# Performance work log

Hardware: AMD Instinct MI355X
Metric: run time of the kernel (lower is better)

Reference implementation:

```python
import jax, jax.numpy as jnp
import numpy as np

B, S, E, H = 256, 64, 256, 8
d = E // H          # qkv_size per head = 32
D = S * d           # flattened per-head linear dim = 2048


def setup_inputs() -> dict:
    key = jax.random.key(0)
    ks = jax.random.split(key, 8)
    w_scale = 1.0 / np.sqrt(D).astype(np.float32)
    return {
        "basic_decoder_out": jax.random.normal(ks[0], (B, S, E), dtype=jnp.float32),
        "final_encoder_out": jax.random.normal(ks[1], (B, S, E), dtype=jnp.float32),
        # stacked per-head Linear params: weight [H, D_out, D_in], bias [H, D_out]
        "WQ": jax.random.normal(ks[2], (H, D, D), dtype=jnp.float32) * w_scale,
        "bQ": jax.random.normal(ks[3], (H, D), dtype=jnp.float32) * w_scale,
        "WK": jax.random.normal(ks[4], (H, D, D), dtype=jnp.float32) * w_scale,
        "bK": jax.random.normal(ks[5], (H, D), dtype=jnp.float32) * w_scale,
        "WV": jax.random.normal(ks[6], (H, D, D), dtype=jnp.float32) * w_scale,
        "bV": jax.random.normal(ks[7], (H, D), dtype=jnp.float32) * w_scale,
    }


def _split_heads_flat(x):
    # [B, S, E] -> [H, B, S*d]: slice head channels, flatten (seq, qkv) per head
    b, s, e = x.shape
    return x.reshape(b, s, H, d).transpose(2, 0, 1, 3).reshape(H, b, s * d)


def reference(basic_decoder_out, final_encoder_out, WQ, bQ, WK, bK, WV, bV):
    b = basic_decoder_out.shape[0]
    xd = _split_heads_flat(basic_decoder_out)   # [H, B, D]
    xe = _split_heads_flat(final_encoder_out)   # [H, B, D]

    # per-head Linear over flattened (seq*qkv): y = x @ W^T + b
    Q = (jnp.einsum('hbi,hoi->hbo', xd, WQ) + bQ[:, None, :]).reshape(H, b, S, d)
    K = (jnp.einsum('hbi,hoi->hbo', xe, WK) + bK[:, None, :]).reshape(H, b, S, d)
    V = (jnp.einsum('hbi,hoi->hbo', xe, WV) + bV[:, None, :]).reshape(H, b, S, d)

    scores = jnp.einsum('hbqd,hbkd->hbqk', Q, K)        # [H, B, Sq, Sk]
    # original uses nn.Softmax(dim=1) on [B, Sq, Sk] -> softmax over QUERY axis
    attn = jax.nn.softmax(scores, axis=2)
    Z = jnp.einsum('hbqk,hbkd->hbqd', attn, V)
    Z = Z * np.float32(1.0 / np.sqrt(d))                # scale applied AFTER attn@V

    # concat heads: [H, B, S, d] -> [B, S, H*d]
    return Z.transpose(1, 2, 0, 3).reshape(b, S, H * d)
```

## Files before the change

### kernel.cpp

```cpp
#include <hip/hip_runtime.h>
#include <hip/hip_fp16.h>

#define HH 8
#define BB 256
#define SS 64
#define EE 256
#define DH 32
#define DD 2048

typedef _Float16 f16x8 __attribute__((ext_vector_type(8)));
typedef _Float16 f16x4 __attribute__((ext_vector_type(4)));
typedef float f32x4v __attribute__((ext_vector_type(4)));

#define BM 256
#define BN 128
#define BK 64
#define LDK 72

__global__ __launch_bounds__(512, 4)
void qkv_kernel(const float* __restrict__ dec, const float* __restrict__ enc,
                const float* __restrict__ WQ, const float* __restrict__ bQ,
                const float* __restrict__ WK, const float* __restrict__ bK,
                const float* __restrict__ WV, const float* __restrict__ bV,
                __half* __restrict__ qkv)
{
    __shared__ _Float16 Asm[BM][LDK];
    __shared__ _Float16 Bsm[BN][LDK];

    const int z = blockIdx.z;
    const int p = z >> 3;
    const int h = z & 7;
    const float* __restrict__ x    = (p == 0) ? dec : enc;
    const float* __restrict__ W    = (p == 0) ? WQ : (p == 1) ? WK : WV;
    const float* __restrict__ bias = (p == 0) ? bQ : (p == 1) ? bK : bV;
    const float* __restrict__ Wh = W + (size_t)h * DD * DD;
    const float* __restrict__ bh = bias + h * DD;
    const int n0 = blockIdx.x * BN;

    const int tid  = threadIdx.x;
    const int lane = tid & 63;
    const int wave = tid >> 6;
    const int wm = wave & 3;
    const int wn = wave >> 2;

    f32x4v acc[4][4];
    #pragma unroll
    for (int m = 0; m < 4; ++m)
        #pragma unroll
        for (int n = 0; n < 4; ++n)
            acc[m][n] = (f32x4v){0.f, 0.f, 0.f, 0.f};

    const int rrow = lane & 15;
    const int kg   = lane >> 4;

    for (int k0 = 0; k0 < DD; k0 += BK) {
        #pragma unroll
        for (int r = 0; r < 8; ++r) {
            int g   = r * 512 + tid;
            int row = g >> 4;
            int k   = (g & 15) * 4;
            const float4 v = *(const float4*)(x + (size_t)row * (SS * EE)
                                + ((k0 + k) >> 5) * EE + h * DH + (k & 31));
            f16x4 hv = { (_Float16)v.x, (_Float16)v.y, (_Float16)v.z, (_Float16)v.w };
            *(f16x4*)&Asm[row][k] = hv;
        }
        #pragma unroll
        for (int r = 0; r < 4; ++r) {
            int g   = r * 512 + tid;
            int row = g >> 4;
            int k   = (g & 15) * 4;
            const float4 v = *(const float4*)(Wh + (size_t)(n0 + row) * DD + k0 + k);
            f16x4 hv = { (_Float16)v.x, (_Float16)v.y, (_Float16)v.z, (_Float16)v.w };
            *(f16x4*)&Bsm[row][k] = hv;
        }
        __syncthreads();

        #pragma unroll
        for (int ks = 0; ks < 2; ++ks) {
            f16x8 af[4], bf[4];
            const int kofs = ks * 32 + kg * 8;
            #pragma unroll
            for (int m = 0; m < 4; ++m)
                af[m] = *(const f16x8*)&Asm[wm * 64 + m * 16 + rrow][kofs];
            #pragma unroll
            for (int n = 0; n < 4; ++n)
                bf[n] = *(const f16x8*)&Bsm[wn * 64 + n * 16 + rrow][kofs];
            #pragma unroll
            for (int m = 0; m < 4; ++m)
                #pragma unroll
                for (int n = 0; n < 4; ++n)
                    acc[m][n] = __builtin_amdgcn_mfma_f32_16x16x32_f16(af[m], bf[n], acc[m][n], 0, 0, 0);
        }
        __syncthreads();
    }

    __half* __restrict__ P = qkv + ((size_t)p * HH + h) * BB * DD;
    const int cg = lane >> 4;
    const int cl = lane & 15;
    #pragma unroll
    for (int n = 0; n < 4; ++n) {
        const int col = n0 + wn * 64 + n * 16 + cl;
        const float bv = bh[col];
        #pragma unroll
        for (int m = 0; m < 4; ++m) {
            const int row = wm * 64 + m * 16 + cg * 4;
            #pragma unroll
            for (int j = 0; j < 4; ++j)
                P[(size_t)(row + j) * DD + col] = (__half)(acc[m][n][j] + bv);
        }
    }
}

__global__ __launch_bounds__(64, 1)
void attn_kernel(const __half* __restrict__ qkv, float* __restrict__ out)
{
    __shared__ float Qf[SS][DH + 4];
    __shared__ float Vf[SS][DH + 4];
    __shared__ float At[SS][SS + 4];

    const int hb = blockIdx.x;
    const int h  = hb >> 8;
    const int b  = hb & 255;
    const int lane = threadIdx.x;

    const __half* __restrict__ Qp = qkv + ((size_t)(0 * HH + h) * BB + b) * DD;
    const __half* __restrict__ Kp = qkv + ((size_t)(1 * HH + h) * BB + b) * DD;
    const __half* __restrict__ Vp = qkv + ((size_t)(2 * HH + h) * BB + b) * DD;

    float kreg[DH];
    {
        const f16x8* kr = (const f16x8*)(Kp + lane * DH);
        #pragma unroll
        for (int i = 0; i < 4; ++i) {
            f16x8 v = kr[i];
            #pragma unroll
            for (int j = 0; j < 8; ++j) kreg[i * 8 + j] = (float)v[j];
        }
        const f16x8* qr = (const f16x8*)(Qp + lane * DH);
        #pragma unroll
        for (int i = 0; i < 4; ++i) {
            f16x8 v = qr[i];
            #pragma unroll
            for (int j = 0; j < 8; ++j) Qf[lane][i * 8 + j] = (float)v[j];
        }
        const f16x8* vr = (const f16x8*)(Vp + lane * DH);
        #pragma unroll
        for (int i = 0; i < 4; ++i) {
            f16x8 v = vr[i];
            #pragma unroll
            for (int j = 0; j < 8; ++j) Vf[lane][i * 8 + j] = (float)v[j];
        }
    }
    __syncthreads();

    float sc[SS];
    #pragma unroll
    for (int q = 0; q < SS; ++q) {
        float s = 0.f;
        #pragma unroll
        for (int d4 = 0; d4 < DH / 4; ++d4) {
            float4 qv = *(const float4*)&Qf[q][d4 * 4];
            s += qv.x * kreg[d4 * 4 + 0] + qv.y * kreg[d4 * 4 + 1]
               + qv.z * kreg[d4 * 4 + 2] + qv.w * kreg[d4 * 4 + 3];
        }
        sc[q] = s;
    }

    float mx = sc[0];
    #pragma unroll
    for (int q = 1; q < SS; ++q) mx = fmaxf(mx, sc[q]);
    float sum = 0.f;
    #pragma unroll
    for (int q = 0; q < SS; ++q) { sc[q] = __expf(sc[q] - mx); sum += sc[q]; }
    const float inv = 0.17677669529663687f / sum;

    #pragma unroll
    for (int q4 = 0; q4 < SS / 4; ++q4) {
        float4 w = { sc[q4 * 4 + 0] * inv, sc[q4 * 4 + 1] * inv,
                     sc[q4 * 4 + 2] * inv, sc[q4 * 4 + 3] * inv };
        *(float4*)&At[lane][q4 * 4] = w;
    }
    __syncthreads();

    float z[DH];
    #pragma unroll
    for (int d = 0; d < DH; ++d) z[d] = 0.f;
    #pragma unroll
    for (int k = 0; k < SS; ++k) {
        const float a = At[k][lane];
        #pragma unroll
        for (int d4 = 0; d4 < DH / 4; ++d4) {
            float4 vv = *(const float4*)&Vf[k][d4 * 4];
            z[d4 * 4 + 0] += a * vv.x;
            z[d4 * 4 + 1] += a * vv.y;
            z[d4 * 4 + 2] += a * vv.z;
            z[d4 * 4 + 3] += a * vv.w;
        }
    }

    float* __restrict__ op = out + (size_t)b * (SS * EE) + (size_t)lane * EE + h * DH;
    #pragma unroll
    for (int d4 = 0; d4 < DH / 4; ++d4) {
        float4 w = { z[d4 * 4 + 0], z[d4 * 4 + 1], z[d4 * 4 + 2], z[d4 * 4 + 3] };
        *(float4*)&op[d4 * 4] = w;
    }
}

extern "C" void kernel_launch(void* const* d_in, const int* in_sizes, int n_in,
                              void* d_out, int out_size, void* d_ws, size_t ws_size,
                              hipStream_t stream)
{
    const float* dec = (const float*)d_in[0];
    const float* enc = (const float*)d_in[1];
    const float* WQ  = (const float*)d_in[2];
    const float* bQ  = (const float*)d_in[3];
    const float* WK  = (const float*)d_in[4];
    const float* bK  = (const float*)d_in[5];
    const float* WV  = (const float*)d_in[6];
    const float* bV  = (const float*)d_in[7];
    __half* qkv = (__half*)d_ws;
    float* out = (float*)d_out;

    dim3 grid1(DD / BN, 1, 3 * HH);
    qkv_kernel<<<grid1, dim3(512, 1, 1), 0, stream>>>(dec, enc, WQ, bQ, WK, bK, WV, bV, qkv);
    attn_kernel<<<dim3(HH * BB, 1, 1), dim3(64, 1, 1), 0, stream>>>(qkv, out);
}
```

Measured before the change: 571.1 us.

## Load QKV weights via direct global-to-LDS, halve N tile, MFMA attention

The projection GEMM now streams fp32 weight tiles straight into LDS with global_load_lds using an XOR swizzle, and converts them to fp16 when reading fragments instead of through registers. The N tile shrinks from 128 to 64 with higher occupancy bounds. The attention kernel is rewritten to compute QK^T and attn@V with MFMA fp16 instructions and a shuffle-based softmax over the query axis. This aims to cut register staging and scalar FMA work, at the cost of more reloading of the activation tile per output column and doubled LDS footprint for fp32 weights.

```diff
diff --git a/kernel.cpp b/kernel.cpp
--- a/kernel.cpp
+++ b/kernel.cpp
@@ -10,14 +10,20 @@
 
 typedef _Float16 f16x8 __attribute__((ext_vector_type(8)));
 typedef _Float16 f16x4 __attribute__((ext_vector_type(4)));
+typedef _Float16 f16x2 __attribute__((ext_vector_type(2)));
 typedef float f32x4v __attribute__((ext_vector_type(4)));
 
 #define BM 256
-#define BN 128
+#define BN 64
 #define BK 64
 #define LDK 72
 
-__global__ __launch_bounds__(512, 4)
+__device__ inline void gload_lds16(const void* g, void* l) {
+    __builtin_amdgcn_global_load_lds((const __attribute__((address_space(1))) void*)g,
+                                     (__attribute__((address_space(3))) void*)l, 16, 0, 0);
+}
+
+__global__ __launch_bounds__(512, 6)
 void qkv_kernel(const float* __restrict__ dec, const float* __restrict__ enc,
                 const float* __restrict__ WQ, const float* __restrict__ bQ,
                 const float* __restrict__ WK, const float* __restrict__ bK,
@@ -25,7 +31,7 @@
                 __half* __restrict__ qkv)
 {
     __shared__ _Float16 Asm[BM][LDK];
-    __shared__ _Float16 Bsm[BN][LDK];
+    __shared__ float    Bsm[BN * BK];
 
     const int z = blockIdx.z;
     const int p = z >> 3;
@@ -43,17 +49,28 @@
     const int wm = wave & 3;
     const int wn = wave >> 2;
 
-    f32x4v acc[4][4];
-    #pragma unroll
-    for (int m = 0; m < 4; ++m)
-        #pragma unroll
-        for (int n = 0; n < 4; ++n)
+    const int r0  = 4 * wave + (lane >> 4);
+    const int cb0 = ((lane & 15) << 4) ^ ((r0 & 7) << 4);
+    const float* gB0 = Wh + (size_t)(n0 + r0) * DD + (cb0 >> 2);
+    const int r1  = 4 * (wave + 8) + (lane >> 4);
+    const int cb1 = ((lane & 15) << 4) ^ ((r1 & 7) << 4);
+    const float* gB1 = Wh + (size_t)(n0 + r1) * DD + (cb1 >> 2);
+    char* ldsB0 = (char*)Bsm + wave * 1024;
+    char* ldsB1 = (char*)Bsm + (wave + 8) * 1024;
+
+    f32x4v acc[4][2];
+    #pragma unroll
+    for (int m = 0; m < 4; ++m)
+        #pragma unroll
+        for (int n = 0; n < 2; ++n)
             acc[m][n] = (f32x4v){0.f, 0.f, 0.f, 0.f};
 
     const int rrow = lane & 15;
     const int kg   = lane >> 4;
 
     for (int k0 = 0; k0 < DD; k0 += BK) {
+        gload_lds16(gB0 + k0, ldsB0);
+        gload_lds16(gB1 + k0, ldsB1);
         #pragma unroll
         for (int r = 0; r < 8; ++r) {
             int g   = r * 512 + tid;
@@ -64,31 +81,33 @@
             f16x4 hv = { (_Float16)v.x, (_Float16)v.y, (_Float16)v.z, (_Float16)v.w };
             *(f16x4*)&Asm[row][k] = hv;
         }
-        #pragma unroll
-        for (int r = 0; r < 4; ++r) {
-            int g   = r * 512 + tid;
-            int row = g >> 4;
-            int k   = (g & 15) * 4;
-            const float4 v = *(const float4*)(Wh + (size_t)(n0 + row) * DD + k0 + k);
-            f16x4 hv = { (_Float16)v.x, (_Float16)v.y, (_Float16)v.z, (_Float16)v.w };
-            *(f16x4*)&Bsm[row][k] = hv;
-        }
         __syncthreads();
 
         #pragma unroll
         for (int ks = 0; ks < 2; ++ks) {
-            f16x8 af[4], bf[4];
             const int kofs = ks * 32 + kg * 8;
+            f16x8 af[4], bf[2];
             #pragma unroll
             for (int m = 0; m < 4; ++m)
                 af[m] = *(const f16x8*)&Asm[wm * 64 + m * 16 + rrow][kofs];
             #pragma unroll
-            for (int n = 0; n < 4; ++n)
-                bf[n] = *(const f16x8*)&Bsm[wn * 64 + n * 16 + rrow][kofs];
+            for (int n = 0; n < 2; ++n) {
+                const int o  = wn * 32 + n * 16 + rrow;
+                const int by = o * 256 + ks * 128 + kg * 32;
+                const int sw = (o & 7) << 4;
+                const float4 lo = *(const float4*)((const char*)Bsm + (by ^ sw));
+                const float4 hi = *(const float4*)((const char*)Bsm + ((by + 16) ^ sw));
+                f16x8 bb;
+                bb[0] = (_Float16)lo.x; bb[1] = (_Float16)lo.y;
+                bb[2] = (_Float16)lo.z; bb[3] = (_Float16)lo.w;
+                bb[4] = (_Float16)hi.x; bb[5] = (_Float16)hi.y;
+                bb[6] = (_Float16)hi.z; bb[7] = (_Float16)hi.w;
+                bf[n] = bb;
+            }
             #pragma unroll
             for (int m = 0; m < 4; ++m)
                 #pragma unroll
-                for (int n = 0; n < 4; ++n)
+                for (int n = 0; n < 2; ++n)
                     acc[m][n] = __builtin_amdgcn_mfma_f32_16x16x32_f16(af[m], bf[n], acc[m][n], 0, 0, 0);
         }
         __syncthreads();
@@ -98,8 +117,8 @@
     const int cg = lane >> 4;
     const int cl = lane & 15;
     #pragma unroll
-    for (int n = 0; n < 4; ++n) {
-        const int col = n0 + wn * 64 + n * 16 + cl;
+    for (int n = 0; n < 2; ++n) {
+        const int col = n0 + wn * 32 + n * 16 + cl;
         const float bv = bh[col];
         #pragma unroll
         for (int m = 0; m < 4; ++m) {
@@ -111,99 +130,119 @@
     }
 }
 
-__global__ __launch_bounds__(64, 1)
+__global__ __launch_bounds__(64)
 void attn_kernel(const __half* __restrict__ qkv, float* __restrict__ out)
 {
-    __shared__ float Qf[SS][DH + 4];
-    __shared__ float Vf[SS][DH + 4];
-    __shared__ float At[SS][SS + 4];
+    __shared__ _Float16 A2[SS][68];
+    __shared__ _Float16 Vt[DH][68];
 
     const int hb = blockIdx.x;
     const int h  = hb >> 8;
     const int b  = hb & 255;
     const int lane = threadIdx.x;
+    const int rrow = lane & 15;
+    const int kg   = lane >> 4;
 
     const __half* __restrict__ Qp = qkv + ((size_t)(0 * HH + h) * BB + b) * DD;
     const __half* __restrict__ Kp = qkv + ((size_t)(1 * HH + h) * BB + b) * DD;
     const __half* __restrict__ Vp = qkv + ((size_t)(2 * HH + h) * BB + b) * DD;
 
-    float kreg[DH];
     {
-        const f16x8* kr = (const f16x8*)(Kp + lane * DH);
-        #pragma unroll
-        for (int i = 0; i < 4; ++i) {
-            f16x8 v = kr[i];
-            #pragma unroll
-            for (int j = 0; j < 8; ++j) kreg[i * 8 + j] = (float)v[j];
-        }
-        const f16x8* qr = (const f16x8*)(Qp + lane * DH);
-        #pragma unroll
-        for (int i = 0; i < 4; ++i) {
-            f16x8 v = qr[i];
-            #pragma unroll
-            for (int j = 0; j < 8; ++j) Qf[lane][i * 8 + j] = (float)v[j];
-        }
         const f16x8* vr = (const f16x8*)(Vp + lane * DH);
         #pragma unroll
         for (int i = 0; i < 4; ++i) {
             f16x8 v = vr[i];
             #pragma unroll
-            for (int j = 0; j < 8; ++j) Vf[lane][i * 8 + j] = (float)v[j];
-        }
-    }
+            for (int j = 0; j < 8; ++j) Vt[i * 8 + j][lane] = v[j];
+        }
+    }
+
+    f32x4v st[4][4];
+    #pragma unroll
+    for (int m = 0; m < 4; ++m)
+        #pragma unroll
+        for (int n = 0; n < 4; ++n)
+            st[m][n] = (f32x4v){0.f, 0.f, 0.f, 0.f};
+    f16x8 kf[4], qf[4];
+    #pragma unroll
+    for (int m = 0; m < 4; ++m)
+        kf[m] = *(const f16x8*)(Kp + (m * 16 + rrow) * DH + kg * 8);
+    #pragma unroll
+    for (int n = 0; n < 4; ++n)
+        qf[n] = *(const f16x8*)(Qp + (n * 16 + rrow) * DH + kg * 8);
+    #pragma unroll
+    for (int m = 0; m < 4; ++m)
+        #pragma unroll
+        for (int n = 0; n < 4; ++n)
+            st[m][n] = __builtin_amdgcn_mfma_f32_16x16x32_f16(kf[m], qf[n], st[m][n], 0, 0, 0);
+
+    #pragma unroll
+    for (int m = 0; m < 4; ++m) {
+        #pragma unroll
+        for (int j = 0; j < 4; ++j) {
+            float v = fmaxf(fmaxf(st[m][0][j], st[m][1][j]),
+                            fmaxf(st[m][2][j], st[m][3][j]));
+            v = fmaxf(v, __shfl_xor(v, 1, 64));
+            v = fmaxf(v, __shfl_xor(v, 2, 64));
+            v = fmaxf(v, __shfl_xor(v, 4, 64));
+            v = fmaxf(v, __shfl_xor(v, 8, 64));
+            float s = 0.f;
+            #pragma unroll
+            for (int n = 0; n < 4; ++n) {
+                float e = __expf(st[m][n][j] - v);
+                st[m][n][j] = e; s += e;
+            }
+            s += __shfl_xor(s, 1, 64);
+            s += __shfl_xor(s, 2, 64);
+            s += __shfl_xor(s, 4, 64);
+            s += __shfl_xor(s, 8, 64);
+            const float inv = 0.17677669529663687f / s;
+            #pragma unroll
+            for (int n = 0; n < 4; ++n) st[m][n][j] *= inv;
+        }
+    }
+    #pragma unroll
+    for (int m = 0; m < 4; ++m)
+        #pragma unroll
+        for (int n = 0; n < 4; ++n) {
+            f16x2 lo, hi;
+            lo[0] = (_Float16)st[m][n][0]; lo[1] = (_Float16)st[m][n][1];
+            hi[0] = (_Float16)st[m][n][2]; hi[1] = (_Float16)st[m][n][3];
+            *(f16x2*)&A2[n * 16 + rrow][m * 16 + kg * 4 + 0] = lo;
+            *(f16x2*)&A2[n * 16 + rrow][m * 16 + kg * 4 + 2] = hi;
+        }
     __syncthreads();
 
-    float sc[SS];
-    #pragma unroll
-    for (int q = 0; q < SS; ++q) {
-        float s = 0.f;
-        #pragma unroll
-        for (int d4 = 0; d4 < DH / 4; ++d4) {
-            float4 qv = *(const float4*)&Qf[q][d4 * 4];
-            s += qv.x * kreg[d4 * 4 + 0] + qv.y * kreg[d4 * 4 + 1]
-               + qv.z * kreg[d4 * 4 + 2] + qv.w * kreg[d4 * 4 + 3];
-        }
-        sc[q] = s;
-    }
-
-    float mx = sc[0];
-    #pragma unroll
-    for (int q = 1; q < SS; ++q) mx = fmaxf(mx, sc[q]);
-    float sum = 0.f;
-    #pragma unroll
-    for (int q = 0; q < SS; ++q) { sc[q] = __expf(sc[q] - mx); sum += sc[q]; }
-    const float inv = 0.17677669529663687f / sum;
-
-    #pragma unroll
-    for (int q4 = 0; q4 < SS / 4; ++q4) {
-        float4 w = { sc[q4 * 4 + 0] * inv, sc[q4 * 4 + 1] * inv,
-                     sc[q4 * 4 + 2] * inv, sc[q4 * 4 + 3] * inv };
-        *(float4*)&At[lane][q4 * 4] = w;
-    }
-    __syncthreads();
-
-    float z[DH];
-    #pragma unroll
-    for (int d = 0; d < DH; ++d) z[d] = 0.f;
-    #pragma unroll
-    for (int k = 0; k < SS; ++k) {
-        const float a = At[k][lane];
-        #pragma unroll
-        for (int d4 = 0; d4 < DH / 4; ++d4) {
-            float4 vv = *(const float4*)&Vf[k][d4 * 4];
-            z[d4 * 4 + 0] += a * vv.x;
-            z[d4 * 4 + 1] += a * vv.y;
-            z[d4 * 4 + 2] += a * vv.z;
-            z[d4 * 4 + 3] += a * vv.w;
-        }
-    }
-
-    float* __restrict__ op = out + (size_t)b * (SS * EE) + (size_t)lane * EE + h * DH;
-    #pragma unroll
-    for (int d4 = 0; d4 < DH / 4; ++d4) {
-        float4 w = { z[d4 * 4 + 0], z[d4 * 4 + 1], z[d4 * 4 + 2], z[d4 * 4 + 3] };
-        *(float4*)&op[d4 * 4] = w;
-    }
+    f32x4v zz[4][2];
+    #pragma unroll
+    for (int m2 = 0; m2 < 4; ++m2)
+        #pragma unroll
+        for (int n2 = 0; n2 < 2; ++n2)
+            zz[m2][n2] = (f32x4v){0.f, 0.f, 0.f, 0.f};
+    #pragma unroll
+    for (int ks = 0; ks < 2; ++ks) {
+        f16x8 pa[4], vb[2];
+        #pragma unroll
+        for (int m2 = 0; m2 < 4; ++m2)
+            pa[m2] = *(const f16x8*)&A2[m2 * 16 + rrow][ks * 32 + kg * 8];
+        #pragma unroll
+        for (int n2 = 0; n2 < 2; ++n2)
+            vb[n2] = *(const f16x8*)&Vt[n2 * 16 + rrow][ks * 32 + kg * 8];
+        #pragma unroll
+        for (int m2 = 0; m2 < 4; ++m2)
+            #pragma unroll
+            for (int n2 = 0; n2 < 2; ++n2)
+                zz[m2][n2] = __builtin_amdgcn_mfma_f32_16x16x32_f16(pa[m2], vb[n2], zz[m2][n2], 0, 0, 0);
+    }
+
+    float* __restrict__ op = out + (size_t)b * (SS * EE) + h * DH;
+    #pragma unroll
+    for (int m2 = 0; m2 < 4; ++m2)
+        #pragma unroll
+        for (int n2 = 0; n2 < 2; ++n2)
+            #pragma unroll
+            for (int j = 0; j < 4; ++j)
+                op[(size_t)(m2 * 16 + kg * 4 + j) * EE + n2 * 16 + rrow] = zz[m2][n2][j];
 }
 
 extern "C" void kernel_launch(void* const* d_in, const int* in_sizes, int n_in,
```

After: 620.2 us. 8.6% more time.
